# Kernel optimization log

Hardware: AMD Instinct MI355X
Metric: run time of the kernel (lower is better)

Reference implementation:

```python
import jax, jax.numpy as jnp
import numpy as np
import math

E = 2048  # embed_dim
H = 16    # num_heads
N = 4     # batch
S = 2048  # target/query length
T = 2048  # source/key length


def setup_inputs() -> dict:
    key = jax.random.key(0)
    ks = jax.random.split(key, 12)
    init = 1.0 / math.sqrt(E)
    inp = {
        "query": jax.random.normal(ks[0], (N, S, E), dtype=jnp.float32),
        "key": jax.random.normal(ks[1], (N, T, E), dtype=jnp.float32),
        "value": jax.random.normal(ks[2], (N, T, E), dtype=jnp.float32),
        "attn_mask": jnp.ones((T, S), dtype=jnp.int32),
        # nn.Linear params, weight shape (out, in)
        "Wq": jax.random.uniform(ks[3], (E, E), jnp.float32, -init, init),
        "bq": jax.random.uniform(ks[4], (E,), jnp.float32, -init, init),
        "Wk": jax.random.uniform(ks[5], (E, E), jnp.float32, -init, init),
        "bk": jax.random.uniform(ks[6], (E,), jnp.float32, -init, init),
        "Wv": jax.random.uniform(ks[7], (E, E), jnp.float32, -init, init),
        "bv": jax.random.uniform(ks[8], (E,), jnp.float32, -init, init),
        "Wp": jax.random.uniform(ks[9], (E, E), jnp.float32, -init, init),
        "bp": jax.random.uniform(ks[10], (E,), jnp.float32, -init, init),
    }
    return inp


def reference(query, key, value, attn_mask, Wq, bq, Wk, bk, Wv, bv, Wp, bp):
    n, s, e = query.shape
    t = key.shape[1]
    d = e // H
    q = (query @ Wq.T + bq).reshape(n, s, H, d)   # (N,S,H,d)
    k = (key @ Wk.T + bk).reshape(n, t, H, d)     # (N,T,H,d)
    v = (value @ Wv.T + bv).reshape(n, t, H, d)   # (N,T,H,d)
    # alignment_swapped in original: (N,H,T,S) with [t,s] = q_s . k_t
    scores = jnp.einsum("nshd,nthd->nhts", q, k)
    scores = jnp.where(attn_mask == 0, -jnp.inf, scores) / jnp.sqrt(jnp.asarray(d, scores.dtype))
    attn = jax.nn.softmax(scores, axis=2)          # softmax over keys t
    # weighted sum over t: out[s] = sum_t attn[t,s] * v[t] -> (N,S,H,d)
    out = jnp.einsum("nhts,nthd->nshd", attn, v).reshape(n, s, e)
    # dropout p=0.0 -> identity
    return out @ Wp.T + bp
```

## Files before the change

kernel.cpp:

```cpp
#include <hip/hip_runtime.h>

#define E_DIM   2048
#define NHEADS  16
#define NBATCH  4
#define SLEN    2048
#define TLEN    2048
#define DHEAD   128
#define MROWS   (NBATCH * SLEN)

typedef __bf16  bf16x8  __attribute__((ext_vector_type(8)));
typedef __bf16  bf16x4  __attribute__((ext_vector_type(4)));
typedef float   floatx4 __attribute__((ext_vector_type(4)));
typedef unsigned short ushort8_v __attribute__((ext_vector_type(8)));

__device__ __forceinline__ unsigned short f2bf(float f) {
    return __builtin_bit_cast(unsigned short, (__bf16)f);
}

__device__ __forceinline__ void gload16(const unsigned short* g, unsigned short* l) {
    __builtin_amdgcn_global_load_lds(
        (const __attribute__((address_space(1))) unsigned int*)(const void*)g,
        (__attribute__((address_space(3))) unsigned int*)(void*)l, 16, 0, 0);
}

__global__ __launch_bounds__(256)
void conv_qkv(const float* __restrict__ q, const float* __restrict__ k,
              const float* __restrict__ v, unsigned short* __restrict__ dst)
{
    const float* src = (blockIdx.y == 0) ? q : ((blockIdx.y == 1) ? k : v);
    const size_t base = (size_t)blockIdx.y * ((size_t)MROWS * E_DIM);
    const size_t i = ((size_t)blockIdx.x * 256 + threadIdx.x) * 8;
    const float4 a = *(const float4*)(src + i);
    const float4 b = *(const float4*)(src + i + 4);
    ushort8_v o;
    o[0]=f2bf(a.x); o[1]=f2bf(a.y); o[2]=f2bf(a.z); o[3]=f2bf(a.w);
    o[4]=f2bf(b.x); o[5]=f2bf(b.y); o[6]=f2bf(b.z); o[7]=f2bf(b.w);
    *(ushort8_v*)(dst + base + i) = o;
}

__global__ __launch_bounds__(256)
void conv_w(const float* __restrict__ w0, const float* __restrict__ w1,
            const float* __restrict__ w2, const float* __restrict__ w3,
            unsigned short* __restrict__ dst)
{
    const float* src = (blockIdx.y == 0) ? w0 : ((blockIdx.y == 1) ? w1 :
                       ((blockIdx.y == 2) ? w2 : w3));
    const size_t base = (size_t)blockIdx.y * ((size_t)E_DIM * E_DIM);
    const size_t i = ((size_t)blockIdx.x * 256 + threadIdx.x) * 8;
    const float4 a = *(const float4*)(src + i);
    const float4 b = *(const float4*)(src + i + 4);
    ushort8_v o;
    o[0]=f2bf(a.x); o[1]=f2bf(a.y); o[2]=f2bf(a.z); o[3]=f2bf(a.w);
    o[4]=f2bf(b.x); o[5]=f2bf(b.y); o[6]=f2bf(b.z); o[7]=f2bf(b.w);
    *(ushort8_v*)(dst + base + i) = o;
}

template<int EPI>
__global__ __launch_bounds__(256, 2)
void gemm_bt(const unsigned short* __restrict__ A, const unsigned short* __restrict__ B,
             const float* __restrict__ bias, void* __restrict__ Cv,
             int M, int Nd, int K, float scale)
{
    __shared__ unsigned short As[128 * 32];
    __shared__ unsigned short Bs[128 * 32];

    const int tid  = threadIdx.x;
    const int bm   = blockIdx.x * 128;
    const int bn   = blockIdx.y * 128;
    const int wave = tid >> 6, lane = tid & 63;
    const int wm   = (wave >> 1) * 64, wn = (wave & 1) * 64;
    const int lrow = lane & 15, quad = lane >> 4;

    const int srow = lane >> 2, schk = lane & 3;
    const int slog = schk ^ ((srow >> 1) & 3);
    const unsigned short* ag = A + (size_t)(bm + wave * 32 + srow) * K + slog * 8;
    const unsigned short* bg = B + (size_t)(bn + wave * 32 + srow) * K + slog * 8;
    unsigned short* lA0 = &As[(wave * 32) * 32];
    unsigned short* lA1 = &As[(wave * 32 + 16) * 32];
    unsigned short* lB0 = &Bs[(wave * 32) * 32];
    unsigned short* lB1 = &Bs[(wave * 32 + 16) * 32];

    const int aswz = (quad ^ ((lrow >> 1) & 3)) * 8;

    floatx4 acc[4][4] = {};

    for (int k0 = 0; k0 < K; k0 += 32) {
        gload16(ag + k0,                  lA0);
        gload16(ag + (size_t)16 * K + k0, lA1);
        gload16(bg + k0,                  lB0);
        gload16(bg + (size_t)16 * K + k0, lB1);
        __syncthreads();

        bf16x8 af[4], bfr[4];
        #pragma unroll
        for (int mi = 0; mi < 4; ++mi)
            af[mi] = *(const bf16x8*)&As[(wm + mi * 16 + lrow) * 32 + aswz];
        #pragma unroll
        for (int ni = 0; ni < 4; ++ni)
            bfr[ni] = *(const bf16x8*)&Bs[(wn + ni * 16 + lrow) * 32 + aswz];
        #pragma unroll
        for (int mi = 0; mi < 4; ++mi)
            #pragma unroll
            for (int ni = 0; ni < 4; ++ni)
                acc[mi][ni] = __builtin_amdgcn_mfma_f32_16x16x32_bf16(af[mi], bfr[ni], acc[mi][ni], 0, 0, 0);
        __syncthreads();
    }

    #pragma unroll
    for (int ni = 0; ni < 4; ++ni) {
        const int col = bn + wn + ni * 16 + lrow;
        const float bv = bias[col];
        #pragma unroll
        for (int mi = 0; mi < 4; ++mi) {
            const int row = bm + wm + mi * 16 + quad * 4;
            if constexpr (EPI == 2) {
                const int n = row >> 11, t = row & 2047;
                const int hh = col >> 7, dd = col & 127;
                unsigned short* dst = (unsigned short*)Cv +
                    (((size_t)(n * 16 + hh) * 128 + dd) * 2048 + t);
                ushort4 w;
                w.x = f2bf((acc[mi][ni][0] + bv) * scale);
                w.y = f2bf((acc[mi][ni][1] + bv) * scale);
                w.z = f2bf((acc[mi][ni][2] + bv) * scale);
                w.w = f2bf((acc[mi][ni][3] + bv) * scale);
                *(ushort4*)dst = w;
            } else {
                #pragma unroll
                for (int i = 0; i < 4; ++i) {
                    const float v = (acc[mi][ni][i] + bv) * scale;
                    if constexpr (EPI == 1)
                        ((unsigned short*)Cv)[(size_t)(row + i) * Nd + col] = f2bf(v);
                    else
                        ((float*)Cv)[(size_t)(row + i) * Nd + col] = v;
                }
            }
        }
    }
}

__global__ __launch_bounds__(256)
void mask_tiles(const int* __restrict__ mask, unsigned char* __restrict__ flags)
{
    __shared__ int s_and, s_or;
    const int tid = threadIdx.x;
    if (tid == 0) { s_and = 1; s_or = 0; }
    __syncthreads();
    const int tt = blockIdx.x >> 4;
    const int ss = blockIdx.x & 15;
    int la = 1, lo = 0;
    #pragma unroll
    for (int it = 0; it < 16; ++it) {
        const int c = it * 256 + tid;
        const int row = c >> 5, c4 = c & 31;
        const int4 v = *(const int4*)(mask + (size_t)(tt * 128 + row) * SLEN + ss * 128 + c4 * 4);
        const int nz = (v.x != 0) + (v.y != 0) + (v.z != 0) + (v.w != 0);
        la &= (nz == 4); lo |= (nz != 0);
    }
    if (!la) atomicAnd(&s_and, 0);
    if (lo)  atomicOr(&s_or, 1);
    __syncthreads();
    if (tid == 0) flags[blockIdx.x] = (unsigned char)(s_and ? 2 : (s_or ? 1 : 0));
}

#define LDP2 40

__global__ __launch_bounds__(256, 2)
void flash_attn(const unsigned short* __restrict__ Q,
                const unsigned short* __restrict__ Kb,
                const unsigned short* __restrict__ Vt,
                const int* __restrict__ mask,
                const unsigned char* __restrict__ tflags,
                unsigned short* __restrict__ O)
{
    __shared__ __align__(16) unsigned short Ks[128 * 128];
    __shared__ __align__(16) unsigned short Vs[128 * 128];
    __shared__ __align__(16) unsigned short Ps[4][32 * LDP2];

    const int tid  = threadIdx.x;
    const int lin  = blockIdx.x + 16 * (blockIdx.y + 16 * blockIdx.z);
    const int nlin = (lin & 7) * 128 + (lin >> 3);
    const int s0   = (nlin & 15) * 128;
    const int h    = (nlin >> 4) & 15;
    const int n    = nlin >> 8;
    const int wave = tid >> 6, lane = tid & 63;
    const int lrow = lane & 15, quad = lane >> 4;
    const int qbase = s0 + wave * 32;

    const int sr4 = lane >> 4;
    const int su  = lane & 15;

    const unsigned short* Kbase = Kb + (size_t)n * TLEN * NHEADS * DHEAD + (size_t)h * DHEAD;
    const unsigned short* Vbase = Vt + ((size_t)(n * NHEADS + h) * DHEAD) * TLEN;

    bf16x8 aq[2][4];
    #pragma unroll
    for (int si = 0; si < 2; ++si)
        #pragma unroll
        for (int kk = 0; kk < 4; ++kk)
            aq[si][kk] = *(const bf16x8*)(Q + ((size_t)(n * SLEN + qbase + si * 16 + lrow) * NHEADS + h) * DHEAD
                                            + kk * 32 + quad * 8);

    float m_r[2] = { -INFINITY, -INFINITY };
    float l_r[2] = { 0.f, 0.f };
    floatx4 occ[2][8] = {};

    for (int t0 = 0; t0 < TLEN; t0 += 128) {
        const int flag = tflags[(t0 >> 7) * (SLEN >> 7) + (s0 >> 7)];
        if (flag == 0) continue;

        #pragma unroll
        for (int i = 0; i < 8; ++i) {
            const int rb = wave * 32 + i * 4;
            const int r  = rb + sr4;
            const int uo = ((su ^ (r & 7)) * 8);
            gload16(Kbase + (size_t)(t0 + r) * (NHEADS * DHEAD) + uo, &Ks[rb * 128]);
            gload16(Vbase + (size_t)r * TLEN + t0 + uo,              &Vs[rb * 128]);
        }
        __syncthreads();

        floatx4 sacc[8][2] = {};
        __builtin_amdgcn_s_setprio(1);
        #pragma unroll
        for (int kk = 0; kk < 4; ++kk)
            #pragma unroll
            for (int ti = 0; ti < 8; ++ti) {
                const bf16x8 ak = *(const bf16x8*)&Ks[(ti * 16 + lrow) * 128
                                                      + ((kk * 4 + quad) ^ (lrow & 7)) * 8];
                sacc[ti][0] = __builtin_amdgcn_mfma_f32_16x16x32_bf16(ak, aq[0][kk], sacc[ti][0], 0, 0, 0);
                sacc[ti][1] = __builtin_amdgcn_mfma_f32_16x16x32_bf16(ak, aq[1][kk], sacc[ti][1], 0, 0, 0);
            }
        __builtin_amdgcn_s_setprio(0);

        if (flag == 1) {
            #pragma unroll
            for (int ti = 0; ti < 8; ++ti)
                #pragma unroll
                for (int si = 0; si < 2; ++si)
                    #pragma unroll
                    for (int i = 0; i < 4; ++i) {
                        const int t = t0 + ti * 16 + quad * 4 + i;
                        const int s = s0 + wave * 32 + si * 16 + lrow;
                        if (mask[(size_t)t * SLEN + s] == 0) sacc[ti][si][i] = -INFINITY;
                    }
        }

        float mt[2];
        #pragma unroll
        for (int si = 0; si < 2; ++si) {
            float v = sacc[0][si][0];
            #pragma unroll
            for (int ti = 0; ti < 8; ++ti)
                #pragma unroll
                for (int i = 0; i < 4; ++i) v = fmaxf(v, sacc[ti][si][i]);
            v = fmaxf(v, __shfl_xor(v, 16));
            v = fmaxf(v, __shfl_xor(v, 32));
            mt[si] = v;
        }

        float alpha[2] = { 1.f, 1.f };
        if (__any((mt[0] > m_r[0] + 8.f) || (mt[1] > m_r[1] + 8.f))) {
            float ao[2][4];
            #pragma unroll
            for (int si = 0; si < 2; ++si) {
                const float mnew = fmaxf(m_r[si], mt[si]);
                alpha[si] = (mnew == -INFINITY) ? 0.f : exp2f(m_r[si] - mnew);
                m_r[si] = mnew;
                #pragma unroll
                for (int i = 0; i < 4; ++i)
                    ao[si][i] = __shfl(alpha[si], quad * 4 + i);
            }
            #pragma unroll
            for (int si = 0; si < 2; ++si)
                #pragma unroll
                for (int nd = 0; nd < 8; ++nd)
                    #pragma unroll
                    for (int i = 0; i < 4; ++i)
                        occ[si][nd][i] *= ao[si][i];
        }
        const float msub[2] = { (m_r[0] == -INFINITY) ? 0.f : m_r[0],
                                (m_r[1] == -INFINITY) ? 0.f : m_r[1] };

        float psum[2] = { 0.f, 0.f };
        #pragma unroll
        for (int kk = 0; kk < 4; ++kk) {
            #pragma unroll
            for (int si = 0; si < 2; ++si)
                #pragma unroll
                for (int half = 0; half < 2; ++half) {
                    const int ti = kk * 2 + half;
                    float p[4];
                    #pragma unroll
                    for (int i = 0; i < 4; ++i)
                        p[i] = exp2f(sacc[ti][si][i] - msub[si]);
                    psum[si] += (p[0] + p[1]) + (p[2] + p[3]);
                    bf16x4 pb;
                    pb[0] = (__bf16)p[0]; pb[1] = (__bf16)p[1];
                    pb[2] = (__bf16)p[2]; pb[3] = (__bf16)p[3];
                    *(bf16x4*)&Ps[wave][(si * 16 + lrow) * LDP2 + half * 16 + quad * 4] = pb;
                }
            bf16x8 ap[2];
            #pragma unroll
            for (int si = 0; si < 2; ++si)
                ap[si] = *(const bf16x8*)&Ps[wave][(si * 16 + lrow) * LDP2 + quad * 8];
            __builtin_amdgcn_s_setprio(1);
            #pragma unroll
            for (int nd = 0; nd < 8; ++nd) {
                const bf16x8 bv = *(const bf16x8*)&Vs[(nd * 16 + lrow) * 128
                                                      + ((kk * 4 + quad) ^ (lrow & 7)) * 8];
                occ[0][nd] = __builtin_amdgcn_mfma_f32_16x16x32_bf16(ap[0], bv, occ[0][nd], 0, 0, 0);
                occ[1][nd] = __builtin_amdgcn_mfma_f32_16x16x32_bf16(ap[1], bv, occ[1][nd], 0, 0, 0);
            }
            __builtin_amdgcn_s_setprio(0);
        }

        #pragma unroll
        for (int si = 0; si < 2; ++si) {
            psum[si] += __shfl_xor(psum[si], 16);
            psum[si] += __shfl_xor(psum[si], 32);
            l_r[si] = l_r[si] * alpha[si] + psum[si];
        }
        __syncthreads();
    }

    float rl[2];
    #pragma unroll
    for (int si = 0; si < 2; ++si)
        rl[si] = (l_r[si] > 0.f) ? 1.0f / l_r[si] : 0.f;
    float rlo[2][4];
    #pragma unroll
    for (int si = 0; si < 2; ++si)
        #pragma unroll
        for (int i = 0; i < 4; ++i)
            rlo[si][i] = __shfl(rl[si], quad * 4 + i);

    #pragma unroll
    for (int si = 0; si < 2; ++si)
        #pragma unroll
        for (int nd = 0; nd < 8; ++nd)
            #pragma unroll
            for (int i = 0; i < 4; ++i) {
                const int srow = s0 + wave * 32 + si * 16 + quad * 4 + i;
                O[((size_t)(n * SLEN + srow) * NHEADS + h) * DHEAD + nd * 16 + lrow] =
                    f2bf(occ[si][nd][i] * rlo[si][i]);
            }
}

extern "C" void kernel_launch(void* const* d_in, const int* in_sizes, int n_in,
                              void* d_out, int out_size, void* d_ws, size_t ws_size,
                              hipStream_t stream)
{
    const float* query = (const float*)d_in[0];
    const float* key   = (const float*)d_in[1];
    const float* value = (const float*)d_in[2];
    const int*   mask  = (const int*)d_in[3];
    const float* Wq = (const float*)d_in[4];  const float* bq = (const float*)d_in[5];
    const float* Wk = (const float*)d_in[6];  const float* bk = (const float*)d_in[7];
    const float* Wv = (const float*)d_in[8];  const float* bv = (const float*)d_in[9];
    const float* Wp = (const float*)d_in[10]; const float* bp = (const float*)d_in[11];
    float* out = (float*)d_out;

    char* ws = (char*)d_ws;
    const size_t SLOT = 32ull * 1024 * 1024;
    unsigned short* Wb  = (unsigned short*)ws;
    unsigned short* Abf = (unsigned short*)(ws + SLOT);
    unsigned short* Bbf = (unsigned short*)(ws + 2 * SLOT);
    unsigned short* Cbf = (unsigned short*)(ws + 3 * SLOT);
    unsigned char*  flags = (unsigned char*)(ws + 4 * SLOT);
    unsigned short* Qb  = (unsigned short*)d_out;
    unsigned short* Kbb = (unsigned short*)((char*)d_out + SLOT);

    const size_t WSLOT = (size_t)E_DIM * E_DIM;
    const dim3 gg(MROWS / 128, E_DIM / 128);
    const float sc = 0.08838834764831845f * 1.4426950408889634f;

    mask_tiles<<<256, 256, 0, stream>>>(mask, flags);
    conv_qkv<<<dim3(8192, 3), 256, 0, stream>>>(query, key, value, Abf);
    conv_w<<<dim3(2048, 4), 256, 0, stream>>>(Wq, Wk, Wv, Wp, Wb);

    gemm_bt<1><<<gg, 256, 0, stream>>>(Abf, Wb,             bq, Qb,  MROWS, E_DIM, E_DIM, sc);
    gemm_bt<1><<<gg, 256, 0, stream>>>(Bbf, Wb + WSLOT,     bk, Kbb, MROWS, E_DIM, E_DIM, 1.f);
    gemm_bt<2><<<gg, 256, 0, stream>>>(Cbf, Wb + 2 * WSLOT, bv, Abf, MROWS, E_DIM, E_DIM, 1.f);
    flash_attn<<<dim3(SLEN / 128, NHEADS, NBATCH), 256, 0, stream>>>(Qb, Kbb, Abf, mask, flags, Cbf);
    gemm_bt<0><<<gg, 256, 0, stream>>>(Cbf, Wb + 3 * WSLOT, bp, out, MROWS, E_DIM, E_DIM, 1.f);
}
```

Baseline: 799.1 us.

## Replace 128x128 GEMM with double-buffered 256x256 tile, 512-thread pipelined kernel

Rewrites the projection GEMM as a 256x256 tile with 8 waves, BK=64, and double-buffered LDS. Global-to-LDS loads for the next K tile are interleaved between four MFMA phases, with explicit vmcnt waits, raw barriers and setprio around the MFMA bursts. The aim is to overlap memory with compute and raise arithmetic intensity per tile. In exchange it uses 128KB of LDS and more accumulator registers, and the grid shrinks to 256 blocks.

```diff
diff --git a/kernel.cpp b/kernel.cpp
--- a/kernel.cpp
+++ b/kernel.cpp
@@ -21,6 +21,12 @@
     __builtin_amdgcn_global_load_lds(
         (const __attribute__((address_space(1))) unsigned int*)(const void*)g,
         (__attribute__((address_space(3))) unsigned int*)(void*)l, 16, 0, 0);
+}
+
+__device__ __forceinline__ void bar() {
+    asm volatile("" ::: "memory");
+    __builtin_amdgcn_s_barrier();
+    asm volatile("" ::: "memory");
 }
 
 __global__ __launch_bounds__(256)
@@ -56,54 +62,123 @@
 }
 
 template<int EPI>
-__global__ __launch_bounds__(256, 2)
-void gemm_bt(const unsigned short* __restrict__ A, const unsigned short* __restrict__ B,
+__global__ __launch_bounds__(512, 2)
+void gemm256(const unsigned short* __restrict__ A, const unsigned short* __restrict__ B,
              const float* __restrict__ bias, void* __restrict__ Cv,
              int M, int Nd, int K, float scale)
 {
-    __shared__ unsigned short As[128 * 32];
-    __shared__ unsigned short Bs[128 * 32];
+    __shared__ unsigned short As[2 * 256 * 64];
+    __shared__ unsigned short Bs[2 * 256 * 64];
 
     const int tid  = threadIdx.x;
-    const int bm   = blockIdx.x * 128;
-    const int bn   = blockIdx.y * 128;
+    const int bm   = blockIdx.x * 256;
+    const int bn   = blockIdx.y * 256;
     const int wave = tid >> 6, lane = tid & 63;
-    const int wm   = (wave >> 1) * 64, wn = (wave & 1) * 64;
+    const int wm   = (wave >> 2) * 128;
+    const int wn   = (wave & 3) * 64;
     const int lrow = lane & 15, quad = lane >> 4;
-
-    const int srow = lane >> 2, schk = lane & 3;
-    const int slog = schk ^ ((srow >> 1) & 3);
-    const unsigned short* ag = A + (size_t)(bm + wave * 32 + srow) * K + slog * 8;
-    const unsigned short* bg = B + (size_t)(bn + wave * 32 + srow) * K + slog * 8;
-    unsigned short* lA0 = &As[(wave * 32) * 32];
-    unsigned short* lA1 = &As[(wave * 32 + 16) * 32];
-    unsigned short* lB0 = &Bs[(wave * 32) * 32];
-    unsigned short* lB1 = &Bs[(wave * 32 + 16) * 32];
-
-    const int aswz = (quad ^ ((lrow >> 1) & 3)) * 8;
-
-    floatx4 acc[4][4] = {};
-
-    for (int k0 = 0; k0 < K; k0 += 32) {
-        gload16(ag + k0,                  lA0);
-        gload16(ag + (size_t)16 * K + k0, lA1);
-        gload16(bg + k0,                  lB0);
-        gload16(bg + (size_t)16 * K + k0, lB1);
-        __syncthreads();
-
-        bf16x8 af[4], bfr[4];
-        #pragma unroll
-        for (int mi = 0; mi < 4; ++mi)
-            af[mi] = *(const bf16x8*)&As[(wm + mi * 16 + lrow) * 32 + aswz];
-        #pragma unroll
-        for (int ni = 0; ni < 4; ++ni)
-            bfr[ni] = *(const bf16x8*)&Bs[(wn + ni * 16 + lrow) * 32 + aswz];
-        #pragma unroll
-        for (int mi = 0; mi < 4; ++mi)
+    const int u0   = (quad ^ (lrow & 7)) * 8;
+    const int u1   = ((4 + quad) ^ (lrow & 7)) * 8;
+
+    const int srow = tid >> 3;
+    const int scol = ((tid & 7) ^ (srow & 7)) * 8;
+    const unsigned short* ag = A + (size_t)(bm + srow) * K + scol;
+    const unsigned short* bg = B + (size_t)(bn + srow) * K + scol;
+    const size_t R64 = (size_t)64 * K, R128 = (size_t)128 * K, R192 = (size_t)192 * K;
+    const int ldsw = wave * 8 * 64;
+
+    floatx4 acc[8][4] = {};
+    const int nt = K / 64;
+
+    gload16(bg,        &Bs[0 * 4096 + ldsw]);
+    gload16(bg + R64,  &Bs[1 * 4096 + ldsw]);
+    gload16(bg + R128, &Bs[2 * 4096 + ldsw]);
+    gload16(bg + R192, &Bs[3 * 4096 + ldsw]);
+    gload16(ag,        &As[0 * 4096 + ldsw]);
+    gload16(ag + R128, &As[2 * 4096 + ldsw]);
+    gload16(ag + R64,  &As[1 * 4096 + ldsw]);
+    gload16(ag + R192, &As[3 * 4096 + ldsw]);
+    asm volatile("s_waitcnt vmcnt(2)" ::: "memory");
+    bar();
+
+    for (int t = 0; t < nt; ++t) {
+        const unsigned short* as = &As[(t & 1) * 16384];
+        const unsigned short* bs = &Bs[(t & 1) * 16384];
+        unsigned short* aD = &As[((t + 1) & 1) * 16384];
+        unsigned short* bD = &Bs[((t + 1) & 1) * 16384];
+        const int k1 = (t + 1) * 64;
+        const bool pf = (t + 1 < nt);
+
+        bf16x8 af[4], bf[4];
+
+        #pragma unroll
+        for (int i = 0; i < 4; ++i)
+            af[i] = *(const bf16x8*)&as[(wm + i * 16 + lrow) * 64 + u0];
+        #pragma unroll
+        for (int i = 0; i < 4; ++i)
+            bf[i] = *(const bf16x8*)&bs[(wn + i * 16 + lrow) * 64 + u0];
+        if (pf) { gload16(bg + k1,       bD + 0 * 4096 + ldsw);
+                  gload16(bg + R64 + k1, bD + 1 * 4096 + ldsw); }
+        bar();
+        __builtin_amdgcn_s_setprio(1);
+        #pragma unroll
+        for (int i = 0; i < 4; ++i)
             #pragma unroll
             for (int ni = 0; ni < 4; ++ni)
-                acc[mi][ni] = __builtin_amdgcn_mfma_f32_16x16x32_bf16(af[mi], bfr[ni], acc[mi][ni], 0, 0, 0);
-        __syncthreads();
+                acc[i][ni] = __builtin_amdgcn_mfma_f32_16x16x32_bf16(af[i], bf[ni], acc[i][ni], 0, 0, 0);
+        __builtin_amdgcn_s_setprio(0);
+        if (pf) asm volatile("s_waitcnt vmcnt(2)" ::: "memory");
+        else    asm volatile("s_waitcnt vmcnt(0)" ::: "memory");
+        bar();
+
+        #pragma unroll
+        for (int i = 0; i < 4; ++i)
+            af[i] = *(const bf16x8*)&as[(wm + 64 + i * 16 + lrow) * 64 + u0];
+        if (pf) { gload16(bg + R128 + k1, bD + 2 * 4096 + ldsw);
+                  gload16(bg + R192 + k1, bD + 3 * 4096 + ldsw); }
+        bar();
+        __builtin_amdgcn_s_setprio(1);
+        #pragma unroll
+        for (int i = 0; i < 4; ++i)
+            #pragma unroll
+            for (int ni = 0; ni < 4; ++ni)
+                acc[4 + i][ni] = __builtin_amdgcn_mfma_f32_16x16x32_bf16(af[i], bf[ni], acc[4 + i][ni], 0, 0, 0);
+        __builtin_amdgcn_s_setprio(0);
+        bar();
+
+        #pragma unroll
+        for (int i = 0; i < 4; ++i)
+            af[i] = *(const bf16x8*)&as[(wm + i * 16 + lrow) * 64 + u1];
+        #pragma unroll
+        for (int i = 0; i < 4; ++i)
+            bf[i] = *(const bf16x8*)&bs[(wn + i * 16 + lrow) * 64 + u1];
+        if (pf) { gload16(ag + k1,        aD + 0 * 4096 + ldsw);
+                  gload16(ag + R128 + k1, aD + 2 * 4096 + ldsw); }
+        bar();
+        __builtin_amdgcn_s_setprio(1);
+        #pragma unroll
+        for (int i = 0; i < 4; ++i)
+            #pragma unroll
+            for (int ni = 0; ni < 4; ++ni)
+                acc[i][ni] = __builtin_amdgcn_mfma_f32_16x16x32_bf16(af[i], bf[ni], acc[i][ni], 0, 0, 0);
+        __builtin_amdgcn_s_setprio(0);
+        bar();
+
+        #pragma unroll
+        for (int i = 0; i < 4; ++i)
+            af[i] = *(const bf16x8*)&as[(wm + 64 + i * 16 + lrow) * 64 + u1];
+        if (pf) { gload16(ag + R64 + k1,  aD + 1 * 4096 + ldsw);
+                  gload16(ag + R192 + k1, aD + 3 * 4096 + ldsw); }
+        bar();
+        __builtin_amdgcn_s_setprio(1);
+        #pragma unroll
+        for (int i = 0; i < 4; ++i)
+            #pragma unroll
+            for (int ni = 0; ni < 4; ++ni)
+                acc[4 + i][ni] = __builtin_amdgcn_mfma_f32_16x16x32_bf16(af[i], bf[ni], acc[4 + i][ni], 0, 0, 0);
+        __builtin_amdgcn_s_setprio(0);
+        if (pf) asm volatile("s_waitcnt vmcnt(2)" ::: "memory");
+        bar();
     }
 
     #pragma unroll
@@ -111,13 +186,13 @@
         const int col = bn + wn + ni * 16 + lrow;
         const float bv = bias[col];
         #pragma unroll
-        for (int mi = 0; mi < 4; ++mi) {
+        for (int mi = 0; mi < 8; ++mi) {
             const int row = bm + wm + mi * 16 + quad * 4;
             if constexpr (EPI == 2) {
-                const int n = row >> 11, t = row & 2047;
+                const int n = row >> 11, tt = row & 2047;
                 const int hh = col >> 7, dd = col & 127;
                 unsigned short* dst = (unsigned short*)Cv +
-                    (((size_t)(n * 16 + hh) * 128 + dd) * 2048 + t);
+                    (((size_t)(n * 16 + hh) * 128 + dd) * 2048 + tt);
                 ushort4 w;
                 w.x = f2bf((acc[mi][ni][0] + bv) * scale);
                 w.y = f2bf((acc[mi][ni][1] + bv) * scale);
@@ -370,16 +445,16 @@
     unsigned short* Kbb = (unsigned short*)((char*)d_out + SLOT);
 
     const size_t WSLOT = (size_t)E_DIM * E_DIM;
-    const dim3 gg(MROWS / 128, E_DIM / 128);
+    const dim3 gg(MROWS / 256, E_DIM / 256);
     const float sc = 0.08838834764831845f * 1.4426950408889634f;
 
     mask_tiles<<<256, 256, 0, stream>>>(mask, flags);
     conv_qkv<<<dim3(8192, 3), 256, 0, stream>>>(query, key, value, Abf);
     conv_w<<<dim3(2048, 4), 256, 0, stream>>>(Wq, Wk, Wv, Wp, Wb);
 
-    gemm_bt<1><<<gg, 256, 0, stream>>>(Abf, Wb,             bq, Qb,  MROWS, E_DIM, E_DIM, sc);
-    gemm_bt<1><<<gg, 256, 0, stream>>>(Bbf, Wb + WSLOT,     bk, Kbb, MROWS, E_DIM, E_DIM, 1.f);
-    gemm_bt<2><<<gg, 256, 0, stream>>>(Cbf, Wb + 2 * WSLOT, bv, Abf, MROWS, E_DIM, E_DIM, 1.f);
+    gemm256<1><<<gg, 512, 0, stream>>>(Abf, Wb,             bq, Qb,  MROWS, E_DIM, E_DIM, sc);
+    gemm256<1><<<gg, 512, 0, stream>>>(Bbf, Wb + WSLOT,     bk, Kbb, MROWS, E_DIM, E_DIM, 1.f);
+    gemm256<2><<<gg, 512, 0, stream>>>(Cbf, Wb + 2 * WSLOT, bv, Abf, MROWS, E_DIM, E_DIM, 1.f);
     flash_attn<<<dim3(SLEN / 128, NHEADS, NBATCH), 256, 0, stream>>>(Qb, Kbb, Abf, mask, flags, Cbf);
-    gemm_bt<0><<<gg, 256, 0, stream>>>(Cbf, Wb + 3 * WSLOT, bp, out, MROWS, E_DIM, E_DIM, 1.f);
-}
+    gemm256<0><<<gg, 512, 0, stream>>>(Cbf, Wb + 3 * WSLOT, bp, out, MROWS, E_DIM, E_DIM, 1.f);
+}
```

New measurement: 784.1 us. No clear change (-1.9%).

## Replace GEMM with 256x256-tile pipelined kernel and fuse K/V projections

Applied to the files above, without the earlier changes.

Replaces the 128x128 GEMM, which did a single-stage LDS load with two barriers per 32-wide K step, with a 512-thread 256x256-tile kernel. The new kernel double-buffers 64-wide K slices via direct global-to-LDS loads, uses explicit vmcnt waits, interleaves loads with MFMA groups and raises wave priority around the MFMAs. The K and V projections are merged into one launch using blockIdx.z, with the epilogue layout chosen at runtime. It aims to hide memory latency and raise MFMA utilisation. In exchange it uses a large LDS footprint that limits occupancy, and the hand-written wait counts must stay exactly right.

```diff
diff --git a/kernel.cpp b/kernel.cpp
--- a/kernel.cpp
+++ b/kernel.cpp
@@ -21,6 +21,12 @@
     __builtin_amdgcn_global_load_lds(
         (const __attribute__((address_space(1))) unsigned int*)(const void*)g,
         (__attribute__((address_space(3))) unsigned int*)(void*)l, 16, 0, 0);
+}
+
+__device__ __forceinline__ void bar() {
+    asm volatile("" ::: "memory");
+    __builtin_amdgcn_s_barrier();
+    asm volatile("" ::: "memory");
 }
 
 __global__ __launch_bounds__(256)
@@ -55,88 +61,178 @@
     *(ushort8_v*)(dst + base + i) = o;
 }
 
+#define GEMM_BODY(EPI_EXPR)                                                          \
+    __shared__ unsigned short As[32768];                                             \
+    __shared__ unsigned short Bs[32768];                                             \
+    const int tid  = threadIdx.x;                                                    \
+    const int bm   = blockIdx.x * 256;                                               \
+    const int bn   = blockIdx.y * 256;                                               \
+    const int wave = tid >> 6, lane = tid & 63;                                      \
+    const int wm   = (wave >> 2) * 128;                                              \
+    const int wn   = (wave & 3) * 64;                                                \
+    const int lrow = lane & 15, quad = lane >> 4;                                    \
+    const int ha   = wm >> 7;                                                        \
+    const int hb   = wn >> 7;                                                        \
+    const int wnr  = wn & 64;                                                        \
+    const int u0   = (quad ^ (lrow & 7)) * 8;                                        \
+    const int u1   = ((4 + quad) ^ (lrow & 7)) * 8;                                  \
+    const int srow = tid >> 3;                                                       \
+    const int scol = ((tid & 7) ^ (srow & 7)) * 8;                                   \
+    const unsigned short* ag = A + (size_t)(bm + srow) * K + scol;                   \
+    const unsigned short* bg = B + (size_t)(bn + srow) * K + scol;                   \
+    const int ldsw = wave * 512;                                                     \
+    floatx4 acc[8][4] = {};                                                          \
+    const int nit = K / 128;                                                         \
+    STG(Bs, bg, 0, 0, 0); STG(Bs, bg, 0, 0, 1);                                      \
+    STG(Bs, bg, 0, 1, 0); STG(Bs, bg, 0, 1, 1);                                      \
+    STG(As, ag, 0, 0, 0); STG(As, ag, 0, 1, 0);                                      \
+    STG(As, ag, 0, 0, 1); STG(As, ag, 0, 1, 1);                                      \
+    STG(Bs, bg, 1, 0, 0); STG(Bs, bg, 1, 0, 1);                                      \
+    STG(Bs, bg, 1, 1, 0); STG(Bs, bg, 1, 1, 1);                                      \
+    STG(As, ag, 1, 0, 0); STG(As, ag, 1, 1, 0);                                      \
+    asm volatile("s_waitcnt vmcnt(6)" ::: "memory");                                 \
+    bar();                                                                           \
+    bf16x8 rb[4][2];                                                                 \
+    for (int it = 0; it < nit; ++it) {                                               \
+        const int O  = 2 * it + 1;                                                   \
+        const int E2 = 2 * it + 2;                                                   \
+        const int O2 = 2 * it + 3;                                                   \
+        const bool pf = (it + 1 < nit);                                              \
+        bf16x8 af[2][2];                                                             \
+        _Pragma("unroll")                                                            \
+        for (int ni = 0; ni < 4; ++ni) { rb[ni][0] = LDB(ni, u0, 0); rb[ni][1] = LDB(ni, u1, 0); } \
+        af[0][0] = LDA(0, u0, 0); af[0][1] = LDA(0, u1, 0);                          \
+        af[1][0] = LDA(1, u0, 0); af[1][1] = LDA(1, u1, 0);                          \
+        STG(As, ag, O, 0, 1); STG(As, ag, O, 1, 1);                                  \
+        bar();                                                                       \
+        MM16(0);                                                                     \
+        bar();                                                                       \
+        af[0][0] = LDA(2, u0, 0); af[0][1] = LDA(2, u1, 0);                          \
+        af[1][0] = LDA(3, u0, 0); af[1][1] = LDA(3, u1, 0);                          \
+        if (pf) { STG(Bs, bg, E2, 0, 0); STG(Bs, bg, E2, 0, 1); }                    \
+        bar();                                                                       \
+        MM16(2);                                                                     \
+        bar();                                                                       \
+        af[0][0] = LDA(4, u0, 0); af[0][1] = LDA(4, u1, 0);                          \
+        af[1][0] = LDA(5, u0, 0); af[1][1] = LDA(5, u1, 0);                          \
+        if (pf) { STG(Bs, bg, E2, 1, 0); STG(Bs, bg, E2, 1, 1); }                    \
+        bar();                                                                       \
+        MM16(4);                                                                     \
+        bar();                                                                       \
+        af[0][0] = LDA(6, u0, 0); af[0][1] = LDA(6, u1, 0);                          \
+        af[1][0] = LDA(7, u0, 0); af[1][1] = LDA(7, u1, 0);                          \
+        if (pf) { STG(As, ag, E2, 0, 0); STG(As, ag, E2, 1, 0); }                    \
+        if (pf) asm volatile("s_waitcnt vmcnt(6)" ::: "memory");                     \
+        else    asm volatile("s_waitcnt vmcnt(0)" ::: "memory");                     \
+        bar();                                                                       \
+        MM16(6);                                                                     \
+        bar();                                                                       \
+        _Pragma("unroll")                                                            \
+        for (int ni = 0; ni < 4; ++ni) { rb[ni][0] = LDB(ni, u0, 1); rb[ni][1] = LDB(ni, u1, 1); } \
+        af[0][0] = LDA(0, u0, 1); af[0][1] = LDA(0, u1, 1);                          \
+        af[1][0] = LDA(1, u0, 1); af[1][1] = LDA(1, u1, 1);                          \
+        if (pf) { STG(As, ag, E2, 0, 1); STG(As, ag, E2, 1, 1); }                    \
+        bar();                                                                       \
+        MM16(0);                                                                     \
+        bar();                                                                       \
+        af[0][0] = LDA(2, u0, 1); af[0][1] = LDA(2, u1, 1);                          \
+        af[1][0] = LDA(3, u0, 1); af[1][1] = LDA(3, u1, 1);                          \
+        if (pf) { STG(Bs, bg, O2, 0, 0); STG(Bs, bg, O2, 0, 1); }                    \
+        bar();                                                                       \
+        MM16(2);                                                                     \
+        bar();                                                                       \
+        af[0][0] = LDA(4, u0, 1); af[0][1] = LDA(4, u1, 1);                          \
+        af[1][0] = LDA(5, u0, 1); af[1][1] = LDA(5, u1, 1);                          \
+        if (pf) { STG(Bs, bg, O2, 1, 0); STG(Bs, bg, O2, 1, 1); }                    \
+        bar();                                                                       \
+        MM16(4);                                                                     \
+        bar();                                                                       \
+        af[0][0] = LDA(6, u0, 1); af[0][1] = LDA(6, u1, 1);                          \
+        af[1][0] = LDA(7, u0, 1); af[1][1] = LDA(7, u1, 1);                          \
+        if (pf) { STG(As, ag, O2, 0, 0); STG(As, ag, O2, 1, 0); }                    \
+        asm volatile("s_waitcnt vmcnt(6)" ::: "memory");                             \
+        bar();                                                                       \
+        MM16(6);                                                                     \
+        bar();                                                                       \
+    }                                                                                \
+    _Pragma("unroll")                                                                \
+    for (int ni = 0; ni < 4; ++ni) {                                                 \
+        const int col = bn + wn + ni * 16 + lrow;                                    \
+        const float bv = bias[col];                                                  \
+        _Pragma("unroll")                                                            \
+        for (int mi = 0; mi < 8; ++mi) {                                             \
+            const int row = bm + wm + mi * 16 + quad * 4;                            \
+            const int epi_ = (EPI_EXPR);                                             \
+            if (epi_ == 2) {                                                         \
+                const int n = row >> 11, tt = row & 2047;                            \
+                const int hh = col >> 7, dd = col & 127;                             \
+                unsigned short* dst = (unsigned short*)Cv +                          \
+                    (((size_t)(n * 16 + hh) * 128 + dd) * 2048 + tt);                \
+                ushort4 w;                                                           \
+                w.x = f2bf((acc[mi][ni][0] + bv) * scale);                           \
+                w.y = f2bf((acc[mi][ni][1] + bv) * scale);                           \
+                w.z = f2bf((acc[mi][ni][2] + bv) * scale);                           \
+                w.w = f2bf((acc[mi][ni][3] + bv) * scale);                           \
+                *(ushort4*)dst = w;                                                  \
+            } else {                                                                 \
+                _Pragma("unroll")                                                    \
+                for (int i = 0; i < 4; ++i) {                                        \
+                    const float v = (acc[mi][ni][i] + bv) * scale;                   \
+                    if (epi_ == 1)                                                   \
+                        ((unsigned short*)Cv)[(size_t)(row + i) * Nd + col] = f2bf(v); \
+                    else                                                             \
+                        ((float*)Cv)[(size_t)(row + i) * Nd + col] = v;              \
+                }                                                                    \
+            }                                                                        \
+        }                                                                            \
+    }
+
+#define STG(Ls, Gp, T, H, S) \
+    gload16((Gp) + (size_t)((H) * 128 + (S) * 64) * K + (size_t)(T) * 64, \
+            (Ls) + (((T) & 1) << 14) + ((H) << 13) + ((S) << 12) + ldsw)
+#define LDA(mi_, u_, s_) (*(const bf16x8*)&As[((s_) << 14) + (ha << 13) + (((mi_) * 16 + lrow) << 6) + (u_)])
+#define LDB(ni_, u_, s_) (*(const bf16x8*)&Bs[((s_) << 14) + (hb << 13) + ((wnr + (ni_) * 16 + lrow) << 6) + (u_)])
+#define MM16(m0) \
+    __builtin_amdgcn_s_setprio(1); \
+    _Pragma("unroll") \
+    for (int ni = 0; ni < 4; ++ni) { \
+        acc[(m0)][ni]     = __builtin_amdgcn_mfma_f32_16x16x32_bf16(af[0][0], rb[ni][0], acc[(m0)][ni], 0, 0, 0); \
+        acc[(m0)][ni]     = __builtin_amdgcn_mfma_f32_16x16x32_bf16(af[0][1], rb[ni][1], acc[(m0)][ni], 0, 0, 0); \
+        acc[(m0) + 1][ni] = __builtin_amdgcn_mfma_f32_16x16x32_bf16(af[1][0], rb[ni][0], acc[(m0) + 1][ni], 0, 0, 0); \
+        acc[(m0) + 1][ni] = __builtin_amdgcn_mfma_f32_16x16x32_bf16(af[1][1], rb[ni][1], acc[(m0) + 1][ni], 0, 0, 0); \
+    } \
+    __builtin_amdgcn_s_setprio(0);
+
 template<int EPI>
-__global__ __launch_bounds__(256, 2)
-void gemm_bt(const unsigned short* __restrict__ A, const unsigned short* __restrict__ B,
+__global__ __launch_bounds__(512, 2)
+void gemm256(const unsigned short* __restrict__ A, const unsigned short* __restrict__ B,
              const float* __restrict__ bias, void* __restrict__ Cv,
              int M, int Nd, int K, float scale)
 {
-    __shared__ unsigned short As[128 * 32];
-    __shared__ unsigned short Bs[128 * 32];
-
-    const int tid  = threadIdx.x;
-    const int bm   = blockIdx.x * 128;
-    const int bn   = blockIdx.y * 128;
-    const int wave = tid >> 6, lane = tid & 63;
-    const int wm   = (wave >> 1) * 64, wn = (wave & 1) * 64;
-    const int lrow = lane & 15, quad = lane >> 4;
-
-    const int srow = lane >> 2, schk = lane & 3;
-    const int slog = schk ^ ((srow >> 1) & 3);
-    const unsigned short* ag = A + (size_t)(bm + wave * 32 + srow) * K + slog * 8;
-    const unsigned short* bg = B + (size_t)(bn + wave * 32 + srow) * K + slog * 8;
-    unsigned short* lA0 = &As[(wave * 32) * 32];
-    unsigned short* lA1 = &As[(wave * 32 + 16) * 32];
-    unsigned short* lB0 = &Bs[(wave * 32) * 32];
-    unsigned short* lB1 = &Bs[(wave * 32 + 16) * 32];
-
-    const int aswz = (quad ^ ((lrow >> 1) & 3)) * 8;
-
-    floatx4 acc[4][4] = {};
-
-    for (int k0 = 0; k0 < K; k0 += 32) {
-        gload16(ag + k0,                  lA0);
-        gload16(ag + (size_t)16 * K + k0, lA1);
-        gload16(bg + k0,                  lB0);
-        gload16(bg + (size_t)16 * K + k0, lB1);
-        __syncthreads();
-
-        bf16x8 af[4], bfr[4];
-        #pragma unroll
-        for (int mi = 0; mi < 4; ++mi)
-            af[mi] = *(const bf16x8*)&As[(wm + mi * 16 + lrow) * 32 + aswz];
-        #pragma unroll
-        for (int ni = 0; ni < 4; ++ni)
-            bfr[ni] = *(const bf16x8*)&Bs[(wn + ni * 16 + lrow) * 32 + aswz];
-        #pragma unroll
-        for (int mi = 0; mi < 4; ++mi)
-            #pragma unroll
-            for (int ni = 0; ni < 4; ++ni)
-                acc[mi][ni] = __builtin_amdgcn_mfma_f32_16x16x32_bf16(af[mi], bfr[ni], acc[mi][ni], 0, 0, 0);
-        __syncthreads();
-    }
-
-    #pragma unroll
-    for (int ni = 0; ni < 4; ++ni) {
-        const int col = bn + wn + ni * 16 + lrow;
-        const float bv = bias[col];
-        #pragma unroll
-        for (int mi = 0; mi < 4; ++mi) {
-            const int row = bm + wm + mi * 16 + quad * 4;
-            if constexpr (EPI == 2) {
-                const int n = row >> 11, t = row & 2047;
-                const int hh = col >> 7, dd = col & 127;
-                unsigned short* dst = (unsigned short*)Cv +
-                    (((size_t)(n * 16 + hh) * 128 + dd) * 2048 + t);
-                ushort4 w;
-                w.x = f2bf((acc[mi][ni][0] + bv) * scale);
-                w.y = f2bf((acc[mi][ni][1] + bv) * scale);
-                w.z = f2bf((acc[mi][ni][2] + bv) * scale);
-                w.w = f2bf((acc[mi][ni][3] + bv) * scale);
-                *(ushort4*)dst = w;
-            } else {
-                #pragma unroll
-                for (int i = 0; i < 4; ++i) {
-                    const float v = (acc[mi][ni][i] + bv) * scale;
-                    if constexpr (EPI == 1)
-                        ((unsigned short*)Cv)[(size_t)(row + i) * Nd + col] = f2bf(v);
-                    else
-                        ((float*)Cv)[(size_t)(row + i) * Nd + col] = v;
-                }
-            }
-        }
-    }
-}
+    GEMM_BODY(EPI)
+}
+
+__global__ __launch_bounds__(512, 2)
+void gemm256_kv(const unsigned short* __restrict__ A0, const unsigned short* __restrict__ A1,
+                const unsigned short* __restrict__ B0, const unsigned short* __restrict__ B1,
+                const float* __restrict__ bias0, const float* __restrict__ bias1,
+                void* __restrict__ C0, void* __restrict__ C1,
+                int M, int Nd, int K)
+{
+    const int z = blockIdx.z;
+    const unsigned short* A = z ? A1 : A0;
+    const unsigned short* B = z ? B1 : B0;
+    const float* bias = z ? bias1 : bias0;
+    void* Cv = z ? C1 : C0;
+    const float scale = 1.f;
+    GEMM_BODY(z ? 2 : 1)
+}
+
+#undef STG
+#undef LDA
+#undef LDB
+#undef MM16
+#undef GEMM_BODY
 
 __global__ __launch_bounds__(256)
 void mask_tiles(const int* __restrict__ mask, unsigned char* __restrict__ flags)
@@ -370,16 +466,16 @@
     unsigned short* Kbb = (unsigned short*)((char*)d_out + SLOT);
 
     const size_t WSLOT = (size_t)E_DIM * E_DIM;
-    const dim3 gg(MROWS / 128, E_DIM / 128);
+    const dim3 gg(MROWS / 256, E_DIM / 256);
     const float sc = 0.08838834764831845f * 1.4426950408889634f;
 
     mask_tiles<<<256, 256, 0, stream>>>(mask, flags);
     conv_qkv<<<dim3(8192, 3), 256, 0, stream>>>(query, key, value, Abf);
     conv_w<<<dim3(2048, 4), 256, 0, stream>>>(Wq, Wk, Wv, Wp, Wb);
 
-    gemm_bt<1><<<gg, 256, 0, stream>>>(Abf, Wb,             bq, Qb,  MROWS, E_DIM, E_DIM, sc);
-    gemm_bt<1><<<gg, 256, 0, stream>>>(Bbf, Wb + WSLOT,     bk, Kbb, MROWS, E_DIM, E_DIM, 1.f);
-    gemm_bt<2><<<gg, 256, 0, stream>>>(Cbf, Wb + 2 * WSLOT, bv, Abf, MROWS, E_DIM, E_DIM, 1.f);
+    gemm256<1><<<gg, 512, 0, stream>>>(Abf, Wb, bq, Qb, MROWS, E_DIM, E_DIM, sc);
+    gemm256_kv<<<dim3(MROWS / 256, E_DIM / 256, 2), 512, 0, stream>>>(
+        Bbf, Cbf, Wb + WSLOT, Wb + 2 * WSLOT, bk, bv, Kbb, Abf, MROWS, E_DIM, E_DIM);
     flash_attn<<<dim3(SLEN / 128, NHEADS, NBATCH), 256, 0, stream>>>(Qb, Kbb, Abf, mask, flags, Cbf);
-    gemm_bt<0><<<gg, 256, 0, stream>>>(Cbf, Wb + 3 * WSLOT, bp, out, MROWS, E_DIM, E_DIM, 1.f);
-}
+    gemm256<0><<<gg, 512, 0, stream>>>(Cbf, Wb + 3 * WSLOT, bp, out, MROWS, E_DIM, E_DIM, 1.f);
+}
```

New measurement: 771.2 us. 1.04x faster.
